# Performance work log

Hardware: AMD Instinct MI355X
Metric: run time of the kernel (lower is better)

Reference implementation:

```python
import jax, jax.numpy as jnp
import numpy as np

EPS = 1e-07

def setup_inputs() -> dict:
    key = jax.random.key(0)
    foreground = jax.random.normal(key, (8, 256, 64, 64), dtype=jnp.float32)
    return {"foreground": foreground}

def reference(foreground):
    bs, ch, h, w = foreground.shape
    # kernels: one 1x1 kernel per spatial position, L2-normalized over channels
    K = foreground.reshape(bs, ch, h * w).transpose(0, 2, 1) + EPS      # [b, hw, c]
    K = K / jnp.sqrt(jnp.sum(K * K, axis=2, keepdims=True))
    # conv2d with 1x1 kernels == per-pixel dot product against every kernel.
    # (padding=patch_size//2 in the torch code is exactly cancelled by the
    #  matching padding of the conv_transpose2d, so it is omitted.)
    scores = jnp.einsum('bkc,bchw->bkhw', K, foreground)                # [b, hw, h, w]
    attn = jax.nn.softmax(scores, axis=1)
    # conv_transpose2d with the same 1x1 kernels == K^T @ attn per pixel
    out = jnp.einsum('bkc,bkhw->bchw', K, attn)                         # [b, c, h, w]
    return out
```

## Files before the change

### kernel.cpp

```cpp
#include <hip/hip_runtime.h>


#define BATCH 8
#define CH 256
#define NPIX 4096
#define EPSV 1e-7f
#define L2E 1.4426950408889634f

using bf16x8 = __attribute__((ext_vector_type(8))) __bf16;
using bf16x4 = __attribute__((ext_vector_type(4))) __bf16;
using f32x4  = __attribute__((ext_vector_type(4))) float;

__device__ __forceinline__ void gload16(const void* g, void* l) {
  __builtin_amdgcn_global_load_lds(
      (const __attribute__((address_space(1))) unsigned int*)g,
      (__attribute__((address_space(3))) unsigned int*)l, 16, 0, 0);
}

__device__ __forceinline__ void barrier_full() {
  asm volatile("s_waitcnt vmcnt(0) lgkmcnt(0)\n"
               "s_barrier" ::: "memory");
}
__device__ __forceinline__ void barrier_lgkm() {
  asm volatile("s_waitcnt lgkmcnt(0)\n"
               "s_barrier" ::: "memory");
}

__global__ __launch_bounds__(256)
void ca_prep(const float* __restrict__ F, __bf16* __restrict__ KA,
             __bf16* __restrict__ KB) {
  const int b   = blockIdx.x;
  const int kt  = blockIdx.y;
  const int kt0 = kt * 32;
  const int t   = threadIdx.x;
  const int k   = t & 31;
  const int h   = (t >> 5) & 1;
  const int w   = t >> 6;

  const float* __restrict__ Fb = F + (size_t)b * CH * NPIX;

  __shared__ float red[4][32];
  __shared__ float invk[32];
  __shared__ __align__(16) __bf16 T[32][264];

  float fv[32];
  float ss = 0.f;
#pragma unroll
  for (int rep = 0; rep < 32; ++rep) {
    int c = rep * 8 + w * 2 + h;
    float v = Fb[(size_t)c * NPIX + kt0 + k] + EPSV;
    fv[rep] = v;
    ss = fmaf(v, v, ss);
  }
  ss += __shfl_xor(ss, 32, 64);
  if ((t & 32) == 0) red[w][k] = ss;
  __syncthreads();
  if (t < 32) invk[t] = rsqrtf(red[0][t] + red[1][t] + red[2][t] + red[3][t]);
  __syncthreads();
  const float iv = invk[k];
#pragma unroll
  for (int rep = 0; rep < 32; ++rep) {
    int c = rep * 8 + w * 2 + h;
    T[k][c] = (__bf16)(fv[rep] * iv);
  }
  __syncthreads();

  __bf16* KAp = KA + ((size_t)b * 128 + kt) * (32 * 256);
#pragma unroll
  for (int pass = 0; pass < 4; ++pass) {
    int kk = pass * 8 + (t >> 5);
    int u  = t & 31;
    bf16x8 v = *(const bf16x8*)&T[kk][u * 8];
    *(bf16x8*)&KAp[kk * 256 + ((u ^ (kk & 7)) * 8)] = v;
  }
  __bf16* KBp = KB + ((size_t)b * 128 + kt) * (256 * 32);
#pragma unroll
  for (int pass = 0; pass < 4; ++pass) {
    int c = pass * 64 + (t >> 2);
    int v = t & 3;
    bf16x8 o;
#pragma unroll
    for (int j = 0; j < 8; ++j) o[j] = T[v * 8 + j][c];
    *(bf16x8*)&KBp[c * 32 + v * 8] = o;
  }
}

__global__ __launch_bounds__(512, 4)
void ca_attn7(const float* __restrict__ F, const __bf16* __restrict__ KA,
              const __bf16* __restrict__ KB, float* __restrict__ Out) {
  __shared__ __align__(16) char smem[81920];

  const int tid  = threadIdx.x;
  const int lane = tid & 63;
  const int w    = tid >> 6;
  const int lq   = lane & 15;
  const int lg   = lane >> 4;
  const int b    = blockIdx.x;
  const int q0   = blockIdx.y * 64;

  const char* KAb = (const char*)(KA + (size_t)b * (size_t)NPIX * CH);
  const char* KBb = (const char*)(KB + (size_t)b * (size_t)NPIX * CH);
  char* PlB = smem + 65536;

  if (w < 4) {
    const int kh = w >> 1, qh = w & 1;
    const int qA = q0 + qh * 32 + lq;
    const int qB = qA + 16;
    const float* __restrict__ Fb = F + (size_t)b * CH * NPIX;
    const int wo = w * 8192;

#pragma unroll
    for (int j = 0; j < 8; ++j)
      gload16(KAb + wo + j * 1024 + lane * 16, smem + wo + j * 1024);

    bf16x8 qfA[8], qfB[8];
    float ssA = 0.f, ssB = 0.f;
#pragma unroll
    for (int cf = 0; cf < 8; ++cf) {
#pragma unroll
      for (int j = 0; j < 8; ++j) {
        int c = cf * 32 + lg * 8 + j;
        float va = Fb[(size_t)c * NPIX + qA];
        float vb = Fb[(size_t)c * NPIX + qB];
        qfA[cf][j] = (__bf16)(va * L2E);
        qfB[cf][j] = (__bf16)(vb * L2E);
        ssA = fmaf(va, va, ssA);
        ssB = fmaf(vb, vb, ssB);
      }
    }
    ssA += __shfl_xor(ssA, 16, 64); ssA += __shfl_xor(ssA, 32, 64);
    ssB += __shfl_xor(ssB, 16, 64); ssB += __shfl_xor(ssB, 32, 64);
    const float mqA = sqrtf(ssA) * L2E, mqB = sqrtf(ssB) * L2E;

    float lA = 0.f, lB = 0.f;
    const int krow = kh * 16 + lq;
    const int ksw  = lq & 7;
    const int rowByte = krow * 512;
    const int pwRowA = (qh * 32 + lq) * 128;
    const int pwRowB = (qh * 32 + 16 + lq) * 128;
    const int puBase = kh * 2 + (lg >> 1);
    const int pwSub  = ((lg & 1) << 3);

    barrier_full();

    const f32x4 zero = {0.f, 0.f, 0.f, 0.f};
    for (int i = 0; i < 64; ++i) {
      const int cb = i & 1;
      if (i < 63) {
        const char* s = KAb + (size_t)(i + 1) * 32768;
        char* d = smem + (cb ^ 1) * 32768;
#pragma unroll
        for (int j = 0; j < 8; ++j)
          gload16(s + wo + j * 1024 + lane * 16, d + wo + j * 1024);
      }

      const char* ab0 = smem + cb * 32768 + rowByte;
      const char* ab1 = ab0 + 16384;
      f32x4 s00 = zero, s01 = zero, s10 = zero, s11 = zero;
      __builtin_amdgcn_s_setprio(1);
#pragma unroll
      for (int cf = 0; cf < 8; ++cf) {
        const int uo = ((((cf << 2) | lg) ^ ksw) << 4);
        bf16x8 a0 = *(const bf16x8*)(ab0 + uo);
        bf16x8 a1 = *(const bf16x8*)(ab1 + uo);
        s00 = __builtin_amdgcn_mfma_f32_16x16x32_bf16(a0, qfA[cf], s00, 0, 0, 0);
        s01 = __builtin_amdgcn_mfma_f32_16x16x32_bf16(a0, qfB[cf], s01, 0, 0, 0);
        s10 = __builtin_amdgcn_mfma_f32_16x16x32_bf16(a1, qfA[cf], s10, 0, 0, 0);
        s11 = __builtin_amdgcn_mfma_f32_16x16x32_bf16(a1, qfB[cf], s11, 0, 0, 0);
      }
      __builtin_amdgcn_s_setprio(0);

      char* pb = PlB + cb * 8192;
      bf16x4 pv00, pv01, pv10, pv11;
#pragma unroll
      for (int r = 0; r < 4; ++r) {
        float p00 = exp2f(s00[r] - mqA);
        float p01 = exp2f(s01[r] - mqB);
        float p10 = exp2f(s10[r] - mqA);
        float p11 = exp2f(s11[r] - mqB);
        lA += p00 + p10; lB += p01 + p11;
        pv00[r] = (__bf16)p00; pv01[r] = (__bf16)p01;
        pv10[r] = (__bf16)p10; pv11[r] = (__bf16)p11;
      }
      {
        const int u0 = (puBase ^ ksw) << 4;
        const int u1 = ((4 + puBase) ^ ksw) << 4;
        *(bf16x4*)(pb + pwRowA + u0 + pwSub) = pv00;
        *(bf16x4*)(pb + pwRowB + u0 + pwSub) = pv01;
        *(bf16x4*)(pb + pwRowA + u1 + pwSub) = pv10;
        *(bf16x4*)(pb + pwRowB + u1 + pwSub) = pv11;
      }

      barrier_full();
    }

    lA += __shfl_xor(lA, 16, 64); lA += __shfl_xor(lA, 32, 64);
    lB += __shfl_xor(lB, 16, 64); lB += __shfl_xor(lB, 32, 64);
    float* lE = (float*)smem;
    if (lg == 0) lE[kh * 64 + qh * 32 + lq] = lA;
    if (lg == 1) lE[kh * 64 + qh * 32 + 16 + lq] = lB;
    barrier_full();

  } else {
    const int cq = w - 4;
    const int c0 = cq * 64;
    const size_t fragBase = (size_t)(c0 + lq) * 64 + (size_t)lg * 16;
    const int prRow = lq * 128;
    const int prU0  = ((0 * 4 + lg) ^ (lq & 7)) << 4;
    const int prU1  = ((1 * 4 + lg) ^ (lq & 7)) << 4;

    const f32x4 zero = {0.f, 0.f, 0.f, 0.f};
    f32x4 oacc[4][4];
#pragma unroll
    for (int i = 0; i < 4; ++i)
#pragma unroll
      for (int j = 0; j < 4; ++j) oacc[i][j] = zero;

    barrier_lgkm();

    for (int jt = 0; jt < 64; ++jt) {
      const char* kb0 = KBb + (size_t)(2 * jt) * 16384 + fragBase;
      const char* kb1 = kb0 + 16384;
      bf16x8 k00 = *(const bf16x8*)(kb0);
      bf16x8 k01 = *(const bf16x8*)(kb0 + 1024);
      bf16x8 k02 = *(const bf16x8*)(kb0 + 2048);
      bf16x8 k03 = *(const bf16x8*)(kb0 + 3072);
      bf16x8 k10 = *(const bf16x8*)(kb1);
      bf16x8 k11 = *(const bf16x8*)(kb1 + 1024);
      bf16x8 k12 = *(const bf16x8*)(kb1 + 2048);
      bf16x8 k13 = *(const bf16x8*)(kb1 + 3072);

      barrier_lgkm();

      const char* pb = PlB + (jt & 1) * 8192;
      __builtin_amdgcn_s_setprio(1);
#pragma unroll
      for (int qf = 0; qf < 4; ++qf) {
        bf16x8 pf0 = *(const bf16x8*)(pb + prRow + qf * 2048 + prU0);
        oacc[0][qf] = __builtin_amdgcn_mfma_f32_16x16x32_bf16(k00, pf0, oacc[0][qf], 0, 0, 0);
        oacc[1][qf] = __builtin_amdgcn_mfma_f32_16x16x32_bf16(k01, pf0, oacc[1][qf], 0, 0, 0);
        oacc[2][qf] = __builtin_amdgcn_mfma_f32_16x16x32_bf16(k02, pf0, oacc[2][qf], 0, 0, 0);
        oacc[3][qf] = __builtin_amdgcn_mfma_f32_16x16x32_bf16(k03, pf0, oacc[3][qf], 0, 0, 0);
      }
#pragma unroll
      for (int qf = 0; qf < 4; ++qf) {
        bf16x8 pf1 = *(const bf16x8*)(pb + prRow + qf * 2048 + prU1);
        oacc[0][qf] = __builtin_amdgcn_mfma_f32_16x16x32_bf16(k10, pf1, oacc[0][qf], 0, 0, 0);
        oacc[1][qf] = __builtin_amdgcn_mfma_f32_16x16x32_bf16(k11, pf1, oacc[1][qf], 0, 0, 0);
        oacc[2][qf] = __builtin_amdgcn_mfma_f32_16x16x32_bf16(k12, pf1, oacc[2][qf], 0, 0, 0);
        oacc[3][qf] = __builtin_amdgcn_mfma_f32_16x16x32_bf16(k13, pf1, oacc[3][qf], 0, 0, 0);
      }
      __builtin_amdgcn_s_setprio(0);
    }

    barrier_lgkm();

    const float* lE = (const float*)smem;
    float rl0 = 1.0f / (lE[0 * 16 + lq] + lE[64 + 0 * 16 + lq]);
    float rl1 = 1.0f / (lE[1 * 16 + lq] + lE[64 + 1 * 16 + lq]);
    float rl2 = 1.0f / (lE[2 * 16 + lq] + lE[64 + 2 * 16 + lq]);
    float rl3 = 1.0f / (lE[3 * 16 + lq] + lE[64 + 3 * 16 + lq]);
    float* __restrict__ Ob = Out + (size_t)b * CH * NPIX;
#pragma unroll
    for (int ct = 0; ct < 4; ++ct) {
#pragma unroll
      for (int r = 0; r < 4; ++r) {
        const int c = c0 + ct * 16 + lg * 4 + r;
        float* orow = Ob + (size_t)c * NPIX + q0;
        orow[0 * 16 + lq] = oacc[ct][0][r] * rl0;
        orow[1 * 16 + lq] = oacc[ct][1][r] * rl1;
        orow[2 * 16 + lq] = oacc[ct][2][r] * rl2;
        orow[3 * 16 + lq] = oacc[ct][3][r] * rl3;
      }
    }
  }
}

extern "C" void kernel_launch(void* const* d_in, const int* in_sizes, int n_in,
                              void* d_out, int out_size, void* d_ws, size_t ws_size,
                              hipStream_t stream) {
  const float* F = (const float*)d_in[0];
  float* out = (float*)d_out;
  const size_t imgElems = (size_t)BATCH * NPIX * CH;

  __bf16* KAi = (__bf16*)d_ws;
  __bf16* KBi = KAi + imgElems;
  ca_prep<<<dim3(BATCH, 128), 256, 0, stream>>>(F, KAi, KBi);
  ca_attn7<<<dim3(BATCH, 64), 512, 0, stream>>>(F, KAi, KBi, out);
}
```

Before: 155.7 us.

## Switch attention kernel MFMAs from 16x16x32 to 32x32x16 tiles

```diff
diff --git a/kernel.cpp b/kernel.cpp
--- a/kernel.cpp
+++ b/kernel.cpp
@@ -10,6 +10,7 @@
 using bf16x8 = __attribute__((ext_vector_type(8))) __bf16;
 using bf16x4 = __attribute__((ext_vector_type(4))) __bf16;
 using f32x4  = __attribute__((ext_vector_type(4))) float;
+using f32x16 = __attribute__((ext_vector_type(16))) float;
 
 __device__ __forceinline__ void gload16(const void* g, void* l) {
   __builtin_amdgcn_global_load_lds(
@@ -86,15 +87,15 @@
 }
 
 __global__ __launch_bounds__(512, 4)
-void ca_attn7(const float* __restrict__ F, const __bf16* __restrict__ KA,
+void ca_attn8(const float* __restrict__ F, const __bf16* __restrict__ KA,
               const __bf16* __restrict__ KB, float* __restrict__ Out) {
   __shared__ __align__(16) char smem[81920];
 
   const int tid  = threadIdx.x;
   const int lane = tid & 63;
   const int w    = tid >> 6;
-  const int lq   = lane & 15;
-  const int lg   = lane >> 4;
+  const int l31  = lane & 31;
+  const int hi   = lane >> 5;
   const int b    = blockIdx.x;
   const int q0   = blockIdx.y * 64;
 
@@ -104,8 +105,7 @@
 
   if (w < 4) {
     const int kh = w >> 1, qh = w & 1;
-    const int qA = q0 + qh * 32 + lq;
-    const int qB = qA + 16;
+    const int qcol = q0 + qh * 32 + l31;
     const float* __restrict__ Fb = F + (size_t)b * CH * NPIX;
     const int wo = w * 8192;
 
@@ -113,37 +113,29 @@
     for (int j = 0; j < 8; ++j)
       gload16(KAb + wo + j * 1024 + lane * 16, smem + wo + j * 1024);
 
-    bf16x8 qfA[8], qfB[8];
-    float ssA = 0.f, ssB = 0.f;
-#pragma unroll
-    for (int cf = 0; cf < 8; ++cf) {
+    bf16x8 qf[16];
+    float ss = 0.f;
+#pragma unroll
+    for (int cs = 0; cs < 16; ++cs) {
 #pragma unroll
       for (int j = 0; j < 8; ++j) {
-        int c = cf * 32 + lg * 8 + j;
-        float va = Fb[(size_t)c * NPIX + qA];
-        float vb = Fb[(size_t)c * NPIX + qB];
-        qfA[cf][j] = (__bf16)(va * L2E);
-        qfB[cf][j] = (__bf16)(vb * L2E);
-        ssA = fmaf(va, va, ssA);
-        ssB = fmaf(vb, vb, ssB);
-      }
-    }
-    ssA += __shfl_xor(ssA, 16, 64); ssA += __shfl_xor(ssA, 32, 64);
-    ssB += __shfl_xor(ssB, 16, 64); ssB += __shfl_xor(ssB, 32, 64);
-    const float mqA = sqrtf(ssA) * L2E, mqB = sqrtf(ssB) * L2E;
-
-    float lA = 0.f, lB = 0.f;
-    const int krow = kh * 16 + lq;
-    const int ksw  = lq & 7;
-    const int rowByte = krow * 512;
-    const int pwRowA = (qh * 32 + lq) * 128;
-    const int pwRowB = (qh * 32 + 16 + lq) * 128;
-    const int puBase = kh * 2 + (lg >> 1);
-    const int pwSub  = ((lg & 1) << 3);
+        int c = cs * 16 + hi * 8 + j;
+        float v = Fb[(size_t)c * NPIX + qcol];
+        qf[cs][j] = (__bf16)(v * L2E);
+        ss = fmaf(v, v, ss);
+      }
+    }
+    ss += __shfl_xor(ss, 32, 64);
+    const float mq = sqrtf(ss) * L2E;
+
+    float lacc = 0.f;
+    const int rowByte = l31 * 512;
+    const int k7 = lane & 7;
+    const int q7 = l31 & 7;
+    const int prow = (qh * 32 + l31) * 128;
 
     barrier_full();
 
-    const f32x4 zero = {0.f, 0.f, 0.f, 0.f};
     for (int i = 0; i < 64; ++i) {
       const int cb = i & 1;
       if (i < 63) {
@@ -154,101 +146,76 @@
           gload16(s + wo + j * 1024 + lane * 16, d + wo + j * 1024);
       }
 
-      const char* ab0 = smem + cb * 32768 + rowByte;
-      const char* ab1 = ab0 + 16384;
-      f32x4 s00 = zero, s01 = zero, s10 = zero, s11 = zero;
+      const char* ab = smem + cb * 32768 + kh * 16384 + rowByte;
+      f32x16 acc = (f32x16)0.0f;
       __builtin_amdgcn_s_setprio(1);
 #pragma unroll
-      for (int cf = 0; cf < 8; ++cf) {
-        const int uo = ((((cf << 2) | lg) ^ ksw) << 4);
-        bf16x8 a0 = *(const bf16x8*)(ab0 + uo);
-        bf16x8 a1 = *(const bf16x8*)(ab1 + uo);
-        s00 = __builtin_amdgcn_mfma_f32_16x16x32_bf16(a0, qfA[cf], s00, 0, 0, 0);
-        s01 = __builtin_amdgcn_mfma_f32_16x16x32_bf16(a0, qfB[cf], s01, 0, 0, 0);
-        s10 = __builtin_amdgcn_mfma_f32_16x16x32_bf16(a1, qfA[cf], s10, 0, 0, 0);
-        s11 = __builtin_amdgcn_mfma_f32_16x16x32_bf16(a1, qfB[cf], s11, 0, 0, 0);
+      for (int cs = 0; cs < 16; ++cs) {
+        bf16x8 a = *(const bf16x8*)(ab + ((((cs << 1) | hi) ^ k7) << 4));
+        acc = __builtin_amdgcn_mfma_f32_32x32x16_bf16(a, qf[cs], acc, 0, 0, 0);
       }
       __builtin_amdgcn_s_setprio(0);
 
       char* pb = PlB + cb * 8192;
-      bf16x4 pv00, pv01, pv10, pv11;
-#pragma unroll
-      for (int r = 0; r < 4; ++r) {
-        float p00 = exp2f(s00[r] - mqA);
-        float p01 = exp2f(s01[r] - mqB);
-        float p10 = exp2f(s10[r] - mqA);
-        float p11 = exp2f(s11[r] - mqB);
-        lA += p00 + p10; lB += p01 + p11;
-        pv00[r] = (__bf16)p00; pv01[r] = (__bf16)p01;
-        pv10[r] = (__bf16)p10; pv11[r] = (__bf16)p11;
-      }
-      {
-        const int u0 = (puBase ^ ksw) << 4;
-        const int u1 = ((4 + puBase) ^ ksw) << 4;
-        *(bf16x4*)(pb + pwRowA + u0 + pwSub) = pv00;
-        *(bf16x4*)(pb + pwRowB + u0 + pwSub) = pv01;
-        *(bf16x4*)(pb + pwRowA + u1 + pwSub) = pv10;
-        *(bf16x4*)(pb + pwRowB + u1 + pwSub) = pv11;
+#pragma unroll
+      for (int g = 0; g < 4; ++g) {
+        bf16x4 pv;
+#pragma unroll
+        for (int s = 0; s < 4; ++s) {
+          float p = __builtin_amdgcn_exp2f(acc[g * 4 + s] - mq);
+          lacc += p;
+          pv[s] = (__bf16)p;
+        }
+        *(bf16x4*)(pb + prow + ((((kh << 2) | g) ^ q7) << 4) + hi * 8) = pv;
       }
 
       barrier_full();
     }
 
-    lA += __shfl_xor(lA, 16, 64); lA += __shfl_xor(lA, 32, 64);
-    lB += __shfl_xor(lB, 16, 64); lB += __shfl_xor(lB, 32, 64);
+    lacc += __shfl_xor(lacc, 32, 64);
     float* lE = (float*)smem;
-    if (lg == 0) lE[kh * 64 + qh * 32 + lq] = lA;
-    if (lg == 1) lE[kh * 64 + qh * 32 + 16 + lq] = lB;
+    if (lane < 32) lE[kh * 64 + qh * 32 + l31] = lacc;
     barrier_full();
 
   } else {
     const int cq = w - 4;
     const int c0 = cq * 64;
-    const size_t fragBase = (size_t)(c0 + lq) * 64 + (size_t)lg * 16;
-    const int prRow = lq * 128;
-    const int prU0  = ((0 * 4 + lg) ^ (lq & 7)) << 4;
-    const int prU1  = ((1 * 4 + lg) ^ (lq & 7)) << 4;
-
-    const f32x4 zero = {0.f, 0.f, 0.f, 0.f};
-    f32x4 oacc[4][4];
-#pragma unroll
-    for (int i = 0; i < 4; ++i)
-#pragma unroll
-      for (int j = 0; j < 4; ++j) oacc[i][j] = zero;
+    const size_t rowByte = (size_t)(c0 + l31) * 64;
+    const int q7 = l31 & 7;
+    const int prow = l31 * 128;
+
+    f32x16 o00 = (f32x16)0.0f, o01 = (f32x16)0.0f;
+    f32x16 o10 = (f32x16)0.0f, o11 = (f32x16)0.0f;
 
     barrier_lgkm();
 
     for (int jt = 0; jt < 64; ++jt) {
-      const char* kb0 = KBb + (size_t)(2 * jt) * 16384 + fragBase;
-      const char* kb1 = kb0 + 16384;
-      bf16x8 k00 = *(const bf16x8*)(kb0);
-      bf16x8 k01 = *(const bf16x8*)(kb0 + 1024);
-      bf16x8 k02 = *(const bf16x8*)(kb0 + 2048);
-      bf16x8 k03 = *(const bf16x8*)(kb0 + 3072);
-      bf16x8 k10 = *(const bf16x8*)(kb1);
-      bf16x8 k11 = *(const bf16x8*)(kb1 + 1024);
-      bf16x8 k12 = *(const bf16x8*)(kb1 + 2048);
-      bf16x8 k13 = *(const bf16x8*)(kb1 + 3072);
+      const char* t0 = KBb + (size_t)(2 * jt) * 16384 + rowByte + hi * 16;
+      const char* t1 = t0 + 16384;
+      bf16x8 kb00 = *(const bf16x8*)(t0);
+      bf16x8 kb01 = *(const bf16x8*)(t0 + 32);
+      bf16x8 kb02 = *(const bf16x8*)(t1);
+      bf16x8 kb03 = *(const bf16x8*)(t1 + 32);
+      bf16x8 kb10 = *(const bf16x8*)(t0 + 2048);
+      bf16x8 kb11 = *(const bf16x8*)(t0 + 2048 + 32);
+      bf16x8 kb12 = *(const bf16x8*)(t1 + 2048);
+      bf16x8 kb13 = *(const bf16x8*)(t1 + 2048 + 32);
 
       barrier_lgkm();
 
       const char* pb = PlB + (jt & 1) * 8192;
       __builtin_amdgcn_s_setprio(1);
 #pragma unroll
-      for (int qf = 0; qf < 4; ++qf) {
-        bf16x8 pf0 = *(const bf16x8*)(pb + prRow + qf * 2048 + prU0);
-        oacc[0][qf] = __builtin_amdgcn_mfma_f32_16x16x32_bf16(k00, pf0, oacc[0][qf], 0, 0, 0);
-        oacc[1][qf] = __builtin_amdgcn_mfma_f32_16x16x32_bf16(k01, pf0, oacc[1][qf], 0, 0, 0);
-        oacc[2][qf] = __builtin_amdgcn_mfma_f32_16x16x32_bf16(k02, pf0, oacc[2][qf], 0, 0, 0);
-        oacc[3][qf] = __builtin_amdgcn_mfma_f32_16x16x32_bf16(k03, pf0, oacc[3][qf], 0, 0, 0);
-      }
-#pragma unroll
-      for (int qf = 0; qf < 4; ++qf) {
-        bf16x8 pf1 = *(const bf16x8*)(pb + prRow + qf * 2048 + prU1);
-        oacc[0][qf] = __builtin_amdgcn_mfma_f32_16x16x32_bf16(k10, pf1, oacc[0][qf], 0, 0, 0);
-        oacc[1][qf] = __builtin_amdgcn_mfma_f32_16x16x32_bf16(k11, pf1, oacc[1][qf], 0, 0, 0);
-        oacc[2][qf] = __builtin_amdgcn_mfma_f32_16x16x32_bf16(k12, pf1, oacc[2][qf], 0, 0, 0);
-        oacc[3][qf] = __builtin_amdgcn_mfma_f32_16x16x32_bf16(k13, pf1, oacc[3][qf], 0, 0, 0);
+      for (int kc = 0; kc < 4; ++kc) {
+        const int uo = ((((kc << 1) | hi) ^ q7) << 4);
+        bf16x8 pf0 = *(const bf16x8*)(pb + prow + uo);
+        bf16x8 pf1 = *(const bf16x8*)(pb + prow + 4096 + uo);
+        bf16x8 k0 = kc == 0 ? kb00 : kc == 1 ? kb01 : kc == 2 ? kb02 : kb03;
+        bf16x8 k1 = kc == 0 ? kb10 : kc == 1 ? kb11 : kc == 2 ? kb12 : kb13;
+        o00 = __builtin_amdgcn_mfma_f32_32x32x16_bf16(k0, pf0, o00, 0, 0, 0);
+        o01 = __builtin_amdgcn_mfma_f32_32x32x16_bf16(k0, pf1, o01, 0, 0, 0);
+        o10 = __builtin_amdgcn_mfma_f32_32x32x16_bf16(k1, pf0, o10, 0, 0, 0);
+        o11 = __builtin_amdgcn_mfma_f32_32x32x16_bf16(k1, pf1, o11, 0, 0, 0);
       }
       __builtin_amdgcn_s_setprio(0);
     }
@@ -256,22 +223,18 @@
     barrier_lgkm();
 
     const float* lE = (const float*)smem;
-    float rl0 = 1.0f / (lE[0 * 16 + lq] + lE[64 + 0 * 16 + lq]);
-    float rl1 = 1.0f / (lE[1 * 16 + lq] + lE[64 + 1 * 16 + lq]);
-    float rl2 = 1.0f / (lE[2 * 16 + lq] + lE[64 + 2 * 16 + lq]);
-    float rl3 = 1.0f / (lE[3 * 16 + lq] + lE[64 + 3 * 16 + lq]);
+    const float rl0 = 1.0f / (lE[l31] + lE[64 + l31]);
+    const float rl1 = 1.0f / (lE[32 + l31] + lE[96 + l31]);
     float* __restrict__ Ob = Out + (size_t)b * CH * NPIX;
 #pragma unroll
-    for (int ct = 0; ct < 4; ++ct) {
-#pragma unroll
-      for (int r = 0; r < 4; ++r) {
-        const int c = c0 + ct * 16 + lg * 4 + r;
-        float* orow = Ob + (size_t)c * NPIX + q0;
-        orow[0 * 16 + lq] = oacc[ct][0][r] * rl0;
-        orow[1 * 16 + lq] = oacc[ct][1][r] * rl1;
-        orow[2 * 16 + lq] = oacc[ct][2][r] * rl2;
-        orow[3 * 16 + lq] = oacc[ct][3][r] * rl3;
-      }
+    for (int r = 0; r < 16; ++r) {
+      const int crow = (r & 3) + 8 * (r >> 2) + 4 * hi;
+      float* orow0 = Ob + (size_t)(c0 + crow) * NPIX + q0;
+      float* orow1 = Ob + (size_t)(c0 + 32 + crow) * NPIX + q0;
+      orow0[l31]      = o00[r] * rl0;
+      orow0[32 + l31] = o01[r] * rl1;
+      orow1[l31]      = o10[r] * rl0;
+      orow1[32 + l31] = o11[r] * rl1;
     }
   }
 }
@@ -286,5 +249,5 @@
   __bf16* KAi = (__bf16*)d_ws;
   __bf16* KBi = KAi + imgElems;
   ca_prep<<<dim3(BATCH, 128), 256, 0, stream>>>(F, KAi, KBi);
-  ca_attn7<<<dim3(BATCH, 64), 512, 0, stream>>>(F, KAi, KBi, out);
-}
+  ca_attn8<<<dim3(BATCH, 64), 512, 0, stream>>>(F, KAi, KBi, out);
+}
```

Result: slower. 161.9 us (+4.0%).

## Double query tile per block to 128 with 16 waves sharing staged K tiles

Applied to the files above, without the earlier changes.

```diff
diff --git a/kernel.cpp b/kernel.cpp
--- a/kernel.cpp
+++ b/kernel.cpp
@@ -85,10 +85,10 @@
   }
 }
 
-__global__ __launch_bounds__(512, 4)
-void ca_attn7(const float* __restrict__ F, const __bf16* __restrict__ KA,
+__global__ __launch_bounds__(1024, 4)
+void ca_attn9(const float* __restrict__ F, const __bf16* __restrict__ KA,
               const __bf16* __restrict__ KB, float* __restrict__ Out) {
-  __shared__ __align__(16) char smem[81920];
+  __shared__ __align__(16) char smem[98304];
 
   const int tid  = threadIdx.x;
   const int lane = tid & 63;
@@ -96,21 +96,21 @@
   const int lq   = lane & 15;
   const int lg   = lane >> 4;
   const int b    = blockIdx.x;
-  const int q0   = blockIdx.y * 64;
+  const int q0   = blockIdx.y * 128;
 
   const char* KAb = (const char*)(KA + (size_t)b * (size_t)NPIX * CH);
   const char* KBb = (const char*)(KB + (size_t)b * (size_t)NPIX * CH);
   char* PlB = smem + 65536;
 
-  if (w < 4) {
-    const int kh = w >> 1, qh = w & 1;
+  if (w < 8) {
+    const int kh = w >> 2, qh = w & 3;
     const int qA = q0 + qh * 32 + lq;
     const int qB = qA + 16;
     const float* __restrict__ Fb = F + (size_t)b * CH * NPIX;
-    const int wo = w * 8192;
-
-#pragma unroll
-    for (int j = 0; j < 8; ++j)
+    const int wo = w * 4096;
+
+#pragma unroll
+    for (int j = 0; j < 4; ++j)
       gload16(KAb + wo + j * 1024 + lane * 16, smem + wo + j * 1024);
 
     bf16x8 qfA[8], qfB[8];
@@ -137,9 +137,11 @@
     const int ksw  = lq & 7;
     const int rowByte = krow * 512;
     const int pwRowA = (qh * 32 + lq) * 128;
-    const int pwRowB = (qh * 32 + 16 + lq) * 128;
+    const int pwRowB = pwRowA + 16 * 128;
     const int puBase = kh * 2 + (lg >> 1);
     const int pwSub  = ((lg & 1) << 3);
+    const int u0 = (puBase ^ ksw) << 4;
+    const int u1 = ((4 + puBase) ^ ksw) << 4;
 
     barrier_full();
 
@@ -150,7 +152,7 @@
         const char* s = KAb + (size_t)(i + 1) * 32768;
         char* d = smem + (cb ^ 1) * 32768;
 #pragma unroll
-        for (int j = 0; j < 8; ++j)
+        for (int j = 0; j < 4; ++j)
           gload16(s + wo + j * 1024 + lane * 16, d + wo + j * 1024);
       }
 
@@ -170,26 +172,22 @@
       }
       __builtin_amdgcn_s_setprio(0);
 
-      char* pb = PlB + cb * 8192;
+      char* pb = PlB + cb * 16384;
       bf16x4 pv00, pv01, pv10, pv11;
 #pragma unroll
       for (int r = 0; r < 4; ++r) {
-        float p00 = exp2f(s00[r] - mqA);
-        float p01 = exp2f(s01[r] - mqB);
-        float p10 = exp2f(s10[r] - mqA);
-        float p11 = exp2f(s11[r] - mqB);
+        float p00 = __builtin_amdgcn_exp2f(s00[r] - mqA);
+        float p01 = __builtin_amdgcn_exp2f(s01[r] - mqB);
+        float p10 = __builtin_amdgcn_exp2f(s10[r] - mqA);
+        float p11 = __builtin_amdgcn_exp2f(s11[r] - mqB);
         lA += p00 + p10; lB += p01 + p11;
         pv00[r] = (__bf16)p00; pv01[r] = (__bf16)p01;
         pv10[r] = (__bf16)p10; pv11[r] = (__bf16)p11;
       }
-      {
-        const int u0 = (puBase ^ ksw) << 4;
-        const int u1 = ((4 + puBase) ^ ksw) << 4;
-        *(bf16x4*)(pb + pwRowA + u0 + pwSub) = pv00;
-        *(bf16x4*)(pb + pwRowB + u0 + pwSub) = pv01;
-        *(bf16x4*)(pb + pwRowA + u1 + pwSub) = pv10;
-        *(bf16x4*)(pb + pwRowB + u1 + pwSub) = pv11;
-      }
+      *(bf16x4*)(pb + pwRowA + u0 + pwSub) = pv00;
+      *(bf16x4*)(pb + pwRowB + u0 + pwSub) = pv01;
+      *(bf16x4*)(pb + pwRowA + u1 + pwSub) = pv10;
+      *(bf16x4*)(pb + pwRowB + u1 + pwSub) = pv11;
 
       barrier_full();
     }
@@ -197,15 +195,16 @@
     lA += __shfl_xor(lA, 16, 64); lA += __shfl_xor(lA, 32, 64);
     lB += __shfl_xor(lB, 16, 64); lB += __shfl_xor(lB, 32, 64);
     float* lE = (float*)smem;
-    if (lg == 0) lE[kh * 64 + qh * 32 + lq] = lA;
-    if (lg == 1) lE[kh * 64 + qh * 32 + 16 + lq] = lB;
+    if (lg == 0) lE[kh * 128 + qh * 32 + lq] = lA;
+    if (lg == 1) lE[kh * 128 + qh * 32 + 16 + lq] = lB;
     barrier_full();
 
   } else {
-    const int cq = w - 4;
-    const int c0 = cq * 64;
+    const int cq  = w - 8;
+    const int c0  = (cq >> 1) * 64;
+    const int qh2 = cq & 1;
     const size_t fragBase = (size_t)(c0 + lq) * 64 + (size_t)lg * 16;
-    const int prRow = lq * 128;
+    const int prRow = (qh2 * 64 + lq) * 128;
     const int prU0  = ((0 * 4 + lg) ^ (lq & 7)) << 4;
     const int prU1  = ((1 * 4 + lg) ^ (lq & 7)) << 4;
 
@@ -232,7 +231,7 @@
 
       barrier_lgkm();
 
-      const char* pb = PlB + (jt & 1) * 8192;
+      const char* pb = PlB + (jt & 1) * 16384;
       __builtin_amdgcn_s_setprio(1);
 #pragma unroll
       for (int qf = 0; qf < 4; ++qf) {
@@ -256,17 +255,18 @@
     barrier_lgkm();
 
     const float* lE = (const float*)smem;
-    float rl0 = 1.0f / (lE[0 * 16 + lq] + lE[64 + 0 * 16 + lq]);
-    float rl1 = 1.0f / (lE[1 * 16 + lq] + lE[64 + 1 * 16 + lq]);
-    float rl2 = 1.0f / (lE[2 * 16 + lq] + lE[64 + 2 * 16 + lq]);
-    float rl3 = 1.0f / (lE[3 * 16 + lq] + lE[64 + 3 * 16 + lq]);
+    const int qb = qh2 * 64;
+    float rl0 = 1.0f / (lE[qb + 0 * 16 + lq] + lE[128 + qb + 0 * 16 + lq]);
+    float rl1 = 1.0f / (lE[qb + 1 * 16 + lq] + lE[128 + qb + 1 * 16 + lq]);
+    float rl2 = 1.0f / (lE[qb + 2 * 16 + lq] + lE[128 + qb + 2 * 16 + lq]);
+    float rl3 = 1.0f / (lE[qb + 3 * 16 + lq] + lE[128 + qb + 3 * 16 + lq]);
     float* __restrict__ Ob = Out + (size_t)b * CH * NPIX;
 #pragma unroll
     for (int ct = 0; ct < 4; ++ct) {
 #pragma unroll
       for (int r = 0; r < 4; ++r) {
         const int c = c0 + ct * 16 + lg * 4 + r;
-        float* orow = Ob + (size_t)c * NPIX + q0;
+        float* orow = Ob + (size_t)c * NPIX + q0 + qb;
         orow[0 * 16 + lq] = oacc[ct][0][r] * rl0;
         orow[1 * 16 + lq] = oacc[ct][1][r] * rl1;
         orow[2 * 16 + lq] = oacc[ct][2][r] * rl2;
@@ -286,5 +286,5 @@
   __bf16* KAi = (__bf16*)d_ws;
   __bf16* KBi = KAi + imgElems;
   ca_prep<<<dim3(BATCH, 128), 256, 0, stream>>>(F, KAi, KBi);
-  ca_attn7<<<dim3(BATCH, 64), 512, 0, stream>>>(F, KAi, KBi, out);
-}
+  ca_attn9<<<dim3(BATCH, 32), 1024, 0, stream>>>(F, KAi, KBi, out);
+}
```

New measurement: 133.1 us. 1.17x faster.
